# Kernel tuning notes

Measured on AMD Instinct MI355X. Metric: run time of the kernel, lower is better.

## Reference

```python
import jax, jax.numpy as jnp
import numpy as np

B = 262144          # flattened batch of (sample, time) points
D = 16              # input_dim: number of independent per-dimension MLPs
TE = 3              # time_embedding_dim -> per-dim MLP input width = 1 + TE = 4
H = 64              # hidden width (model_dims = [64, 64, 1])


def setup_inputs() -> dict:
    key = jax.random.key(0)
    ks = jax.random.split(key, 8)
    s1 = 1.0 / np.sqrt(1 + TE)   # torch nn.Linear default init scale ~ U(-1/sqrt(fan_in), ...)
    s2 = 1.0 / np.sqrt(H)
    return {
        "t": jax.random.normal(ks[0], (B, TE), jnp.float32),
        "y": jax.random.normal(ks[1], (B, D), jnp.float32),
        # stacked per-dim weights: layer l weight [D, in_l, out_l], bias [D, out_l]
        "W1": jax.random.uniform(ks[2], (D, 1 + TE, H), jnp.float32, -s1, s1),
        "b1": jax.random.uniform(ks[3], (D, H), jnp.float32, -s1, s1),
        "W2": jax.random.uniform(ks[4], (D, H, H), jnp.float32, -s2, s2),
        "b2": jax.random.uniform(ks[5], (D, H), jnp.float32, -s2, s2),
        "W3": jax.random.uniform(ks[6], (D, H, 1), jnp.float32, -s2, s2),
        "b3": jax.random.uniform(ks[7], (D, 1), jnp.float32, -s2, s2),
    }


def reference(t, y, W1, b1, W2, b2, W3, b3):
    # Per-dim MLP input: concat([y_i, t]) -> [B, D, 1+TE]
    Bn, Dn = y.shape
    x = jnp.concatenate(
        [y[:, :, None], jnp.broadcast_to(t[:, None, :], (Bn, Dn, t.shape[-1]))], axis=-1
    )
    h = jax.nn.softplus(jnp.einsum("bdi,dih->bdh", x, W1) + b1)      # Linear + Softplus
    h = jax.nn.softplus(jnp.einsum("bdh,dhk->bdk", h, W2) + b2)      # Linear + Softplus
    out = jnp.einsum("bdk,dko->bdo", h, W3) + b3                      # final Linear, out=1
    # concat over D then final activation: [B, D]
    return jax.nn.softplus(out[..., 0])
```

## Files before the change

### kernel.cpp

```cpp
#include <hip/hip_runtime.h>
#include <cmath>

#define B_TOTAL 262144
#define D 16
#define TE 3
#define H 64

#define TPB 16
#define NBX (B_TOTAL / 16 / TPB)
#define NBY 4

#define LOG2E 1.44269504088896340736f
#define LN2   0.693147180559945309417f

#define RSH 72
#define ARS 10

typedef _Float16 half8  __attribute__((ext_vector_type(8)));
typedef _Float16 half4  __attribute__((ext_vector_type(4)));
typedef __fp16   fp16x2 __attribute__((ext_vector_type(2)));
typedef float    f32x4  __attribute__((ext_vector_type(4)));
typedef unsigned int uint32;

__device__ __forceinline__ float sp_log2(float xs) {
    return __builtin_amdgcn_logf(1.0f + __builtin_amdgcn_exp2f(xs));
}
__device__ __forceinline__ float softplus_full(float x) {
    float e = __builtin_amdgcn_exp2f(-fabsf(x) * LOG2E);
    return fmaxf(x, 0.0f) + LN2 * __builtin_amdgcn_logf(1.0f + e);
}

__global__ __launch_bounds__(256, 5) void DiagonalVariance_kernel(
    const float* __restrict__ t,
    const float* __restrict__ y,
    const float* __restrict__ W1,
    const float* __restrict__ b1,
    const float* __restrict__ W2,
    const float* __restrict__ b2,
    const float* __restrict__ W3,
    const float* __restrict__ b3,
    float* __restrict__ out)
{
    __shared__ __align__(16) _Float16 tbuf[4 * 16 * RSH];
    __shared__ __align__(16) float obuf[TPB * 16 * 4];
    __shared__ __align__(16) uint32 abuf[256 * ARS];

    const int wave = threadIdx.x >> 6;
    const int lane = threadIdx.x & 63;
    const int q    = lane >> 4;
    const int lm   = lane & 15;
    const int d    = blockIdx.y * 4 + wave;
    const bool q0  = (q == 0);

    {
        const int i    = threadIdx.x;
        const int grow = blockIdx.x * 256 + i;
        const f32x4 yv = *(const f32x4*)(y + grow * D + blockIdx.y * 4);
        const float* tpp = t + grow * TE;
        const float tt0 = tpp[0], tt1 = tpp[1], tt2 = tpp[2];
        const uint32 u1 = __builtin_bit_cast(uint32, __builtin_amdgcn_cvt_pkrtz(tt1, tt2));
        uint32* ab = abuf + i * ARS;
        ab[0] = __builtin_bit_cast(uint32, __builtin_amdgcn_cvt_pkrtz(yv.x, tt0)); ab[1] = u1;
        ab[2] = __builtin_bit_cast(uint32, __builtin_amdgcn_cvt_pkrtz(yv.y, tt0)); ab[3] = u1;
        ab[4] = __builtin_bit_cast(uint32, __builtin_amdgcn_cvt_pkrtz(yv.z, tt0)); ab[5] = u1;
        ab[6] = __builtin_bit_cast(uint32, __builtin_amdgcn_cvt_pkrtz(yv.w, tt0)); ab[7] = u1;
    }

    const float* __restrict__ W1d = W1 + d * (4 * H);
    const float* __restrict__ b1d = b1 + d * H;
    const float* __restrict__ W2d = W2 + d * (H * H);
    const float* __restrict__ b2d = b2 + d * H;
    const float* __restrict__ W3d = W3 + d * H;

    half8 w2f[2][4];
    #pragma unroll
    for (int ks = 0; ks < 2; ++ks)
        #pragma unroll
        for (int nt = 0; nt < 4; ++nt)
            #pragma unroll
            for (int j = 0; j < 8; ++j)
                w2f[ks][nt][j] = (_Float16)W2d[(32 * ks + 8 * q + j) * H + 16 * nt + lm];

    half4 w1f[4];
    #pragma unroll
    for (int nt = 0; nt < 4; ++nt) {
        #pragma unroll
        for (int i = 0; i < 4; ++i) {
            const int h = 16 * nt + lm;
            float v = 0.0f;
            if (q == 0)           v = W1d[i * H + h] * LOG2E;
            if (q == 1 && i == 0) v = b1d[h] * LOG2E;
            w1f[nt][i] = (_Float16)v;
        }
    }

    half8 w3f[2];
    #pragma unroll
    for (int ks = 0; ks < 2; ++ks)
        #pragma unroll
        for (int j = 0; j < 8; ++j)
            w3f[ks][j] = (_Float16)(W3d[32 * ks + 8 * q + j] * LN2);

    float b2s[4];
    #pragma unroll
    for (int nt = 0; nt < 4; ++nt)
        b2s[nt] = b2d[16 * nt + lm] * LOG2E;
    const float b3v = b3[d];

    _Float16* const tb  = tbuf + wave * (16 * RSH);
    _Float16* const twr = tb + (q * 4) * RSH + lm;
    const _Float16* const trd = tb + lm * RSH + 8 * q;

    const uint32* const ard = abuf + lm * ARS + 2 * wave;

    __syncthreads();

    #pragma unroll 1
    for (int tg = 0; tg < TPB; ++tg) {
        const uint32 a0 = ard[tg * 16 * ARS + 0];
        const uint32 a1 = ard[tg * 16 * ARS + 1];
        union { half4 h; uint32 u[2]; } af;
        af.u[0] = q0 ? a0 : 0x00003C00u;
        af.u[1] = q0 ? a1 : 0u;

        f32x4 acc1[4];
        #pragma unroll
        for (int nt = 0; nt < 4; ++nt)
            acc1[nt] = __builtin_amdgcn_mfma_f32_16x16x16f16(
                af.h, w1f[nt], (f32x4){0.f, 0.f, 0.f, 0.f}, 0, 0, 0);

        #pragma unroll
        for (int nt = 0; nt < 4; ++nt)
            #pragma unroll
            for (int r = 0; r < 4; ++r)
                twr[r * RSH + nt * 16] = (_Float16)sp_log2(acc1[nt][r]);

        half8 a2[2];
        #pragma unroll
        for (int ks = 0; ks < 2; ++ks)
            a2[ks] = *(const half8*)(trd + 32 * ks);

        f32x4 acc2[4];
        #pragma unroll
        for (int nt = 0; nt < 4; ++nt)
            acc2[nt] = __builtin_amdgcn_mfma_f32_16x16x32_f16(
                a2[0], w2f[0][nt], (f32x4){0.f, 0.f, 0.f, 0.f}, 0, 0, 0);
        #pragma unroll
        for (int nt = 0; nt < 4; ++nt)
            acc2[nt] = __builtin_amdgcn_mfma_f32_16x16x32_f16(a2[1], w2f[1][nt], acc2[nt], 0, 0, 0);

        #pragma unroll
        for (int nt = 0; nt < 4; ++nt)
            #pragma unroll
            for (int r = 0; r < 4; ++r)
                twr[r * RSH + nt * 16] = (_Float16)sp_log2(acc2[nt][r] + b2s[nt]);

        half8 a3[2];
        #pragma unroll
        for (int ks = 0; ks < 2; ++ks)
            a3[ks] = *(const half8*)(trd + 32 * ks);

        f32x4 acc3;
        acc3 = __builtin_amdgcn_mfma_f32_16x16x32_f16(a3[0], w3f[0], (f32x4){0.f, 0.f, 0.f, 0.f}, 0, 0, 0);
        acc3 = __builtin_amdgcn_mfma_f32_16x16x32_f16(a3[1], w3f[1], acc3, 0, 0, 0);

        const float v01 = (lm & 1) ? acc3[1] : acc3[0];
        const float v23 = (lm & 1) ? acc3[3] : acc3[2];
        const float vs  = (lm & 2) ? v23 : v01;
        if (lm < 4)
            obuf[(tg * 16 + q * 4 + lm) * 4 + wave] = softplus_full(vs + b3v);
    }

    __syncthreads();
    const int i = threadIdx.x;
    const f32x4 v = *(const f32x4*)(obuf + 4 * i);
    *(f32x4*)(out + (blockIdx.x * 256 + i) * D + blockIdx.y * 4) = v;
}

extern "C" void kernel_launch(void* const* d_in, const int* in_sizes, int n_in,
                              void* d_out, int out_size, void* d_ws, size_t ws_size,
                              hipStream_t stream) {
    const float* t  = (const float*)d_in[0];
    const float* y  = (const float*)d_in[1];
    const float* W1 = (const float*)d_in[2];
    const float* b1 = (const float*)d_in[3];
    const float* W2 = (const float*)d_in[4];
    const float* b2 = (const float*)d_in[5];
    const float* W3 = (const float*)d_in[6];
    const float* b3 = (const float*)d_in[7];
    float* out = (float*)d_out;

    DiagonalVariance_kernel<<<dim3(NBX, NBY), dim3(256), 0, stream>>>(
        t, y, W1, b1, W2, b2, W3, b3, out);
}
```

Before: 209.4 us.

## Replace softplus log with polynomial, fold b2 into MFMA accumulator, raise occupancy

Replaces the exp2+log softplus with one exp2 followed by a cubic polynomial approximation of log1p(e) on e in (0,1]. The hidden-layer version works in the log2-scaled domain, and the final softplus gets its own coefficients. The layer-2 bias is now used as the initial MFMA accumulator instead of being added afterwards, and the launch-bounds occupancy hint goes from 5 to 6. This removes a transcendental op per element and some VALU adds, at the cost of approximation error in the activations and possibly more register pressure from the vector bias.

```diff
diff --git a/kernel.cpp b/kernel.cpp
--- a/kernel.cpp
+++ b/kernel.cpp
@@ -22,15 +22,33 @@
 typedef float    f32x4  __attribute__((ext_vector_type(4)));
 typedef unsigned int uint32;
 
-__device__ __forceinline__ float sp_log2(float xs) {
-    return __builtin_amdgcn_logf(1.0f + __builtin_amdgcn_exp2f(xs));
-}
-__device__ __forceinline__ float softplus_full(float x) {
-    float e = __builtin_amdgcn_exp2f(-fabsf(x) * LOG2E);
-    return fmaxf(x, 0.0f) + LN2 * __builtin_amdgcn_logf(1.0f + e);
-}
-
-__global__ __launch_bounds__(256, 5) void DiagonalVariance_kernel(
+#define PA 1.4426950f
+#define PB -0.7096327f
+#define PC 0.3894332f
+#define PD -0.1224955f
+#define QA 1.0f
+#define QB -0.4919312f
+#define QC 0.2699534f
+#define QD -0.0849116f
+
+__device__ __forceinline__ float sp_poly(float x) {
+    const float m = fmaxf(x, 0.0f);
+    const float e = __builtin_amdgcn_exp2f(-fabsf(x));
+    float p = fmaf(e, PD, PC);
+    p = fmaf(e, p, PB);
+    p = fmaf(e, p, PA);
+    return fmaf(e, p, m);
+}
+__device__ __forceinline__ float softplus_final(float x) {
+    const float m = fmaxf(x, 0.0f);
+    const float e = __builtin_amdgcn_exp2f(-fabsf(x) * LOG2E);
+    float p = fmaf(e, QD, QC);
+    p = fmaf(e, p, QB);
+    p = fmaf(e, p, QA);
+    return fmaf(e, p, m);
+}
+
+__global__ __launch_bounds__(256, 6) void DiagonalVariance_kernel(
     const float* __restrict__ t,
     const float* __restrict__ y,
     const float* __restrict__ W1,
@@ -101,10 +119,12 @@
         for (int j = 0; j < 8; ++j)
             w3f[ks][j] = (_Float16)(W3d[32 * ks + 8 * q + j] * LN2);
 
-    float b2s[4];
-    #pragma unroll
-    for (int nt = 0; nt < 4; ++nt)
-        b2s[nt] = b2d[16 * nt + lm] * LOG2E;
+    f32x4 b2f[4];
+    #pragma unroll
+    for (int nt = 0; nt < 4; ++nt) {
+        const float bv = b2d[16 * nt + lm] * LOG2E;
+        b2f[nt] = (f32x4){bv, bv, bv, bv};
+    }
     const float b3v = b3[d];
 
     _Float16* const tb  = tbuf + wave * (16 * RSH);
@@ -133,7 +153,7 @@
         for (int nt = 0; nt < 4; ++nt)
             #pragma unroll
             for (int r = 0; r < 4; ++r)
-                twr[r * RSH + nt * 16] = (_Float16)sp_log2(acc1[nt][r]);
+                twr[r * RSH + nt * 16] = (_Float16)sp_poly(acc1[nt][r]);
 
         half8 a2[2];
         #pragma unroll
@@ -143,8 +163,7 @@
         f32x4 acc2[4];
         #pragma unroll
         for (int nt = 0; nt < 4; ++nt)
-            acc2[nt] = __builtin_amdgcn_mfma_f32_16x16x32_f16(
-                a2[0], w2f[0][nt], (f32x4){0.f, 0.f, 0.f, 0.f}, 0, 0, 0);
+            acc2[nt] = __builtin_amdgcn_mfma_f32_16x16x32_f16(a2[0], w2f[0][nt], b2f[nt], 0, 0, 0);
         #pragma unroll
         for (int nt = 0; nt < 4; ++nt)
             acc2[nt] = __builtin_amdgcn_mfma_f32_16x16x32_f16(a2[1], w2f[1][nt], acc2[nt], 0, 0, 0);
@@ -153,7 +172,7 @@
         for (int nt = 0; nt < 4; ++nt)
             #pragma unroll
             for (int r = 0; r < 4; ++r)
-                twr[r * RSH + nt * 16] = (_Float16)sp_log2(acc2[nt][r] + b2s[nt]);
+                twr[r * RSH + nt * 16] = (_Float16)sp_poly(acc2[nt][r]);
 
         half8 a3[2];
         #pragma unroll
@@ -168,7 +187,7 @@
         const float v23 = (lm & 1) ? acc3[3] : acc3[2];
         const float vs  = (lm & 2) ? v23 : v01;
         if (lm < 4)
-            obuf[(tg * 16 + q * 4 + lm) * 4 + wave] = softplus_full(vs + b3v);
+            obuf[(tg * 16 + q * 4 + lm) * 4 + wave] = softplus_final(vs + b3v);
     }
 
     __syncthreads();
```

Measured after the change: 293.9 us. 40.4% more time.
